# Kernel tuning notes

Hardware: AMD Instinct MI355X
Metric: run time of the kernel (lower is better)

The kernel has to match this reference:

```python
import jax, jax.numpy as jnp
import numpy as np
from jax import lax

HEADS = 4
DIM_HEAD = 32
IH = IW = 64
IH_RED = 32  # image_size // reduce_ratio; F.interpolate(size=int) -> square output


def dw_conv(t, w):
    # depthwise 3x3, stride 1, padding 1, NCHW; w: [C,1,3,3]
    return lax.conv_general_dilated(t, w, (1, 1), [(1, 1), (1, 1)],
                                    feature_group_count=t.shape[1],
                                    dimension_numbers=("NCHW", "OIHW", "NCHW"))


def pw_conv(t, w):
    # pointwise 1x1 conv as einsum; w: [O,C,1,1]
    return jnp.einsum("oc,bchw->bohw", w[:, :, 0, 0], t)


def resize_bilinear_ac(t, out_h, out_w):
    # bilinear, align_corners=True, t: [B,C,H,W]
    H, W = t.shape[-2], t.shape[-1]
    ys = jnp.linspace(0.0, H - 1.0, out_h)
    xs = jnp.linspace(0.0, W - 1.0, out_w)
    y0 = jnp.floor(ys).astype(jnp.int32)
    x0 = jnp.floor(xs).astype(jnp.int32)
    y1 = jnp.minimum(y0 + 1, H - 1)
    x1 = jnp.minimum(x0 + 1, W - 1)
    wy = (ys - y0).astype(t.dtype)[None, None, :, None]
    wx = (xs - x0).astype(t.dtype)[None, None, None, :]
    row = t[:, :, y0, :] * (1 - wy) + t[:, :, y1, :] * wy  # [B,C,OH,W]
    out = row[:, :, :, x0] * (1 - wx) + row[:, :, :, x1] * wx  # [B,C,OH,OW]
    return out


def to_heads(t):
    # [B, h*d, H, W] -> [B, h, H*W, d]
    B, _, H, W = t.shape
    return t.reshape(B, HEADS, DIM_HEAD, H * W).transpose(0, 1, 3, 2)


def setup_inputs() -> dict:
    key = jax.random.key(0)
    ks = jax.random.split(key, 7)
    inner = HEADS * DIM_HEAD  # 128
    return {
        "x": jax.random.normal(ks[0], (8, 256, 16, 16), jnp.float32),
        "skip": jax.random.normal(ks[1], (8, 128, 64, 64), jnp.float32),
        "dw_q": jax.random.normal(ks[2], (128, 1, 3, 3), jnp.float32) * 0.1,
        "pw_q": jax.random.normal(ks[3], (inner, 128, 1, 1), jnp.float32) * 0.05,
        "dw_kv": jax.random.normal(ks[4], (256, 1, 3, 3), jnp.float32) * 0.1,
        "pw_kv": jax.random.normal(ks[5], (2 * inner, 256, 1, 1), jnp.float32) * 0.05,
        "w_out": jax.random.normal(ks[6], (128, inner, 1, 1), jnp.float32) * 0.05,
    }


def reference(x, skip, dw_q, pw_q, dw_kv, pw_kv, w_out):
    scale = DIM_HEAD ** -0.5
    q = to_heads(pw_conv(dw_conv(skip, dw_q), pw_q))  # [B,h,4096,d]
    kv = pw_conv(dw_conv(x, dw_kv), pw_kv)            # [B,2*inner,16,16]
    k, v = jnp.split(kv, 2, axis=1)
    k = to_heads(resize_bilinear_ac(k, IH_RED, IH_RED))  # [B,h,1024,d]
    v = to_heads(resize_bilinear_ac(v, IH_RED, IH_RED))
    dots = jnp.einsum("bhqd,bhkd->bhqk", q, k) * scale
    attn = jax.nn.softmax(dots, axis=-1)
    out = jnp.einsum("bhqk,bhkd->bhqd", attn, v)  # [B,h,4096,d]
    B = out.shape[0]
    out = out.transpose(0, 1, 3, 2).reshape(B, HEADS * DIM_HEAD, IH, IW)
    return pw_conv(out, w_out)
```

## Files before the change

kernel.cpp:

```cpp
#include <hip/hip_runtime.h>
#include <hip/hip_bf16.h>

typedef __attribute__((ext_vector_type(4))) float f32x4;
typedef __attribute__((ext_vector_type(8))) short bf16x8;

#define DEV static __device__ __forceinline__

DEV int imin(int a, int b) { return a < b ? a : b; }

DEV short f2bf(float f) {
  union { float f; unsigned u; } v; v.f = f;
  unsigned r = (v.u + 0x7fffu + ((v.u >> 16) & 1u)) >> 16;
  return (short)r;
}

DEV unsigned pkbf(float lo, float hi) {
  unsigned r;
  asm("v_cvt_pk_bf16_f32 %0, %1, %2" : "=v"(r) : "v"(lo), "v"(hi));
  return r;
}

DEV bf16x8 cvt8(const float* __restrict__ p) {
  f32x4 a = *reinterpret_cast<const f32x4*>(p);
  f32x4 b = *reinterpret_cast<const f32x4*>(p + 4);
  bf16x8 r;
  r[0] = f2bf(a[0]); r[1] = f2bf(a[1]); r[2] = f2bf(a[2]); r[3] = f2bf(a[3]);
  r[4] = f2bf(b[0]); r[5] = f2bf(b[1]); r[6] = f2bf(b[2]); r[7] = f2bf(b[3]);
  return r;
}

DEV int swz(int q, int c) {
  return q * 64 + ((((c >> 1) ^ (q & 3)) << 4) | ((c & 1) << 3));
}
DEV int swz_rd(int q, int pair) {
  return q * 64 + ((pair ^ (q & 3)) << 4);
}

__global__ __launch_bounds__(256) void k_dwq(const float* __restrict__ skip,
    const float* __restrict__ dw_q, short* __restrict__ dwQ) {
  const int b = blockIdx.z, cq = blockIdx.y, y = blockIdx.x;
  __shared__ __align__(16) short T[64][40];
  const int t = threadIdx.x;
  {
    const int x = t & 63, cg = t >> 6;
    #pragma unroll
    for (int i = 0; i < 8; ++i) {
      const int cl = cg * 8 + i;
      const int c = cq * 32 + cl;
      const float* sp = skip + (b * 128 + c) * 4096;
      const float* wp = dw_q + c * 9;
      float acc = 0.f;
      #pragma unroll
      for (int ky = 0; ky < 3; ++ky) {
        const int yy = y + ky - 1;
        if (yy < 0 || yy > 63) continue;
        #pragma unroll
        for (int kx = 0; kx < 3; ++kx) {
          const int xx = x + kx - 1;
          if (xx < 0 || xx > 63) continue;
          acc += sp[yy * 64 + xx] * wp[ky * 3 + kx];
        }
      }
      T[x][cl] = f2bf(acc);
    }
  }
  __syncthreads();
  const int x2 = t >> 2, cc = t & 3;
  bf16x8 v = *reinterpret_cast<const bf16x8*>(&T[x2][cc * 8]);
  *reinterpret_cast<bf16x8*>(dwQ + (b * 4096 + y * 64 + x2) * 128 + cq * 32 + cc * 8) = v;
}

__global__ __launch_bounds__(256) void k_kvgen(const float* __restrict__ x,
    const float* __restrict__ dw_kv, const float* __restrict__ pw_kv,
    float* __restrict__ kv16) {
  const int b = blockIdx.y;
  const int pq = blockIdx.x;
  __shared__ __align__(16) short dwxT[16][264];
  const int t = threadIdx.x;
  {
    const int pl = t & 15;
    const int cg = t >> 4;
    const int py = pq, px = pl;
    for (int i = 0; i < 16; ++i) {
      const int c = cg * 16 + i;
      const float* sp = x + (b * 256 + c) * 256;
      const float* wp = dw_kv + c * 9;
      float acc = 0.f;
      #pragma unroll
      for (int ky = 0; ky < 3; ++ky) {
        const int yy = py + ky - 1;
        if (yy < 0 || yy > 15) continue;
        #pragma unroll
        for (int kx = 0; kx < 3; ++kx) {
          const int xx = px + kx - 1;
          if (xx < 0 || xx > 15) continue;
          acc += sp[yy * 16 + xx] * wp[ky * 3 + kx];
        }
      }
      dwxT[pl][c] = f2bf(acc);
    }
  }
  __syncthreads();
  const int w = t >> 6, l = t & 63, lr = l & 15, lg = l >> 4;
  f32x4 acc[4];
  #pragma unroll
  for (int ot = 0; ot < 4; ++ot) acc[ot] = f32x4{0.f, 0.f, 0.f, 0.f};
  #pragma unroll
  for (int kk = 0; kk < 8; ++kk) {
    const int c0 = kk * 32 + lg * 8;
    bf16x8 bfr = *reinterpret_cast<const bf16x8*>(&dwxT[lr][c0]);
    #pragma unroll
    for (int ot = 0; ot < 4; ++ot) {
      const int o = (w * 4 + ot) * 16 + lr;
      bf16x8 afr = cvt8(pw_kv + o * 256 + c0);
      acc[ot] = __builtin_amdgcn_mfma_f32_16x16x32_bf16(afr, bfr, acc[ot], 0, 0, 0);
    }
  }
  #pragma unroll
  for (int ot = 0; ot < 4; ++ot)
    #pragma unroll
    for (int r = 0; r < 4; ++r) {
      const int o = (w * 4 + ot) * 16 + lg * 4 + r;
      const int pix = pq * 16 + lr;
      kv16[(b * 256 + o) * 256 + pix] = acc[ot][r];
    }
}

DEV float bilin16(const float* __restrict__ p, int key) {
  const int oy = key >> 5, ox = key & 31;
  const float s = 15.f / 31.f;
  const float syf = oy * s, sxf = ox * s;
  const int y0 = (int)syf, x0 = (int)sxf;
  const int y1 = imin(y0 + 1, 15), x1 = imin(x0 + 1, 15);
  const float wy = syf - (float)y0, wx = sxf - (float)x0;
  const float r0 = p[y0 * 16 + x0] * (1.f - wx) + p[y0 * 16 + x1] * wx;
  const float r1 = p[y1 * 16 + x0] * (1.f - wx) + p[y1 * 16 + x1] * wx;
  return r0 * (1.f - wy) + r1 * wy;
}

__global__ __launch_bounds__(256) void k_resize(const float* __restrict__ kv16,
    short* __restrict__ K, short* __restrict__ Vt) {
  const int idx = blockIdx.x * 256 + threadIdx.x;
  {
    const int d = idx & 31;
    int rest = idx >> 5;
    const int key = rest & 1023; rest >>= 10;
    const int h = rest & 3; const int b = rest >> 2;
    const int ch = h * 32 + d;
    K[idx] = f2bf(bilin16(kv16 + (b * 256 + ch) * 256, key));
  }
  {
    const int key = idx & 1023;
    int rest = idx >> 10;
    const int d = rest & 31; rest >>= 5;
    const int h = rest & 3; const int b = rest >> 2;
    const int ch = 128 + h * 32 + d;
    Vt[idx] = f2bf(bilin16(kv16 + (b * 256 + ch) * 256, key));
  }
}

__global__ __launch_bounds__(256) void k_attn(const short* __restrict__ dwQ,
    const float* __restrict__ pw_q, const short* __restrict__ Kk,
    const short* __restrict__ Vt, const float* __restrict__ w_out,
    float* __restrict__ out) {
  const int b = blockIdx.y;
  const int q0 = blockIdx.x * 32;
  const int t = threadIdx.x, h = t >> 6, l = t & 63;
  const int lr = l & 15, lg = l >> 4;
  __shared__ __align__(16) short QT[32][136];
  __shared__ __align__(16) char QS[4][2048];
  __shared__ __align__(16) char PS[4][1024];
  __shared__ __align__(16) short AT[32][136];

  {
    const int rr = t >> 4, c16 = t & 15;
    #pragma unroll
    for (int i = 0; i < 2; ++i) {
      const int q = rr + i * 16;
      bf16x8 v = *reinterpret_cast<const bf16x8*>(dwQ + (b * 4096 + q0 + q) * 128 + c16 * 8);
      *reinterpret_cast<bf16x8*>(&QT[q][c16 * 8]) = v;
    }
  }
  __syncthreads();

  {
    f32x4 aq[2][2];
    #pragma unroll
    for (int ot = 0; ot < 2; ++ot)
      #pragma unroll
      for (int qt = 0; qt < 2; ++qt) aq[ot][qt] = f32x4{0.f, 0.f, 0.f, 0.f};
    #pragma unroll
    for (int kk = 0; kk < 4; ++kk) {
      const int c0 = kk * 32 + lg * 8;
      bf16x8 bfr[2];
      #pragma unroll
      for (int qt = 0; qt < 2; ++qt)
        bfr[qt] = *reinterpret_cast<const bf16x8*>(&QT[qt * 16 + lr][c0]);
      #pragma unroll
      for (int ot = 0; ot < 2; ++ot) {
        bf16x8 afr = cvt8(pw_q + ((h * 2 + ot) * 16 + lr) * 128 + c0);
        #pragma unroll
        for (int qt = 0; qt < 2; ++qt)
          aq[ot][qt] = __builtin_amdgcn_mfma_f32_16x16x32_bf16(afr, bfr[qt], aq[ot][qt], 0, 0, 0);
      }
    }
    const float qs = 0.25505403f;
    #pragma unroll
    for (int ot = 0; ot < 2; ++ot)
      #pragma unroll
      for (int qt = 0; qt < 2; ++qt) {
        unsigned d0 = pkbf(aq[ot][qt][0] * qs, aq[ot][qt][1] * qs);
        unsigned d1 = pkbf(aq[ot][qt][2] * qs, aq[ot][qt][3] * qs);
        const int q = qt * 16 + lr, c = ot * 4 + lg;
        *reinterpret_cast<unsigned long long*>(QS[h] + swz(q, c)) =
            ((unsigned long long)d1 << 32) | d0;
      }
  }
  asm volatile("s_waitcnt lgkmcnt(0)" ::: "memory");
  __builtin_amdgcn_sched_barrier(0);
  bf16x8 qf[2];
  #pragma unroll
  for (int qt = 0; qt < 2; ++qt) {
    const int q = qt * 16 + lr;
    qf[qt] = *reinterpret_cast<const bf16x8*>(QS[h] + swz_rd(q, lg));
  }
  __builtin_amdgcn_sched_barrier(0);

  const short* Kb = Kk + (b * 4 + h) * 32768;
  const short* Vb = Vt + (b * 4 + h) * 32768;
  f32x4 oacc[2][2];
  float ls[2];
  #pragma unroll
  for (int qt = 0; qt < 2; ++qt) {
    oacc[qt][0] = f32x4{0.f, 0.f, 0.f, 0.f};
    oacc[qt][1] = f32x4{0.f, 0.f, 0.f, 0.f};
    ls[qt] = 0.f;
  }
  for (int kc = 0; kc < 1024; kc += 32) {
    bf16x8 kf[2], vf[2];
    #pragma unroll
    for (int tt = 0; tt < 2; ++tt) {
      kf[tt] = *reinterpret_cast<const bf16x8*>(Kb + (kc + tt * 16 + lr) * 32 + lg * 8);
      vf[tt] = *reinterpret_cast<const bf16x8*>(Vb + (tt * 16 + lr) * 1024 + kc + lg * 8);
    }
    #pragma unroll
    for (int qt = 0; qt < 2; ++qt) {
      const f32x4 z = f32x4{0.f, 0.f, 0.f, 0.f};
      f32x4 s0 = __builtin_amdgcn_mfma_f32_16x16x32_bf16(kf[0], qf[qt], z, 0, 0, 0);
      f32x4 s1 = __builtin_amdgcn_mfma_f32_16x16x32_bf16(kf[1], qf[qt], z, 0, 0, 0);
      float p0[4], p1[4];
      #pragma unroll
      for (int r = 0; r < 4; ++r) {
        p0[r] = __builtin_amdgcn_exp2f(s0[r]);
        p1[r] = __builtin_amdgcn_exp2f(s1[r]);
      }
      ls[qt] += ((p0[0] + p0[1]) + (p0[2] + p0[3])) + ((p1[0] + p1[1]) + (p1[2] + p1[3]));
      unsigned a0 = pkbf(p0[0], p0[1]), a1 = pkbf(p0[2], p0[3]);
      unsigned b0 = pkbf(p1[0], p1[1]), b1 = pkbf(p1[2], p1[3]);
      *reinterpret_cast<unsigned long long*>(PS[h] + swz(lr, lg)) =
          ((unsigned long long)a1 << 32) | a0;
      *reinterpret_cast<unsigned long long*>(PS[h] + swz(lr, lg + 4)) =
          ((unsigned long long)b1 << 32) | b0;
      asm volatile("s_waitcnt lgkmcnt(0)" ::: "memory");
      __builtin_amdgcn_sched_barrier(0);
      bf16x8 pf = *reinterpret_cast<const bf16x8*>(PS[h] + swz_rd(lr, lg));
      __builtin_amdgcn_sched_barrier(0);
      oacc[qt][0] = __builtin_amdgcn_mfma_f32_16x16x32_bf16(pf, vf[0], oacc[qt][0], 0, 0, 0);
      oacc[qt][1] = __builtin_amdgcn_mfma_f32_16x16x32_bf16(pf, vf[1], oacc[qt][1], 0, 0, 0);
    }
  }

  #pragma unroll
  for (int qt = 0; qt < 2; ++qt) {
    float s = ls[qt];
    s += __shfl_xor(s, 16);
    s += __shfl_xor(s, 32);
    const float inv = 1.f / s;
    #pragma unroll
    for (int r = 0; r < 4; ++r) {
      const float invr = __shfl(inv, lg * 4 + r);
      const int q = qt * 16 + lg * 4 + r;
      #pragma unroll
      for (int tt = 0; tt < 2; ++tt)
        AT[q][h * 32 + tt * 16 + lr] = f2bf(oacc[qt][tt][r] * invr);
    }
  }
  __syncthreads();

  f32x4 ao[2][2];
  #pragma unroll
  for (int jt = 0; jt < 2; ++jt)
    #pragma unroll
    for (int qt = 0; qt < 2; ++qt) ao[jt][qt] = f32x4{0.f, 0.f, 0.f, 0.f};
  #pragma unroll
  for (int kk = 0; kk < 4; ++kk) {
    const int c0 = kk * 32 + lg * 8;
    bf16x8 bfr[2];
    #pragma unroll
    for (int qt = 0; qt < 2; ++qt)
      bfr[qt] = *reinterpret_cast<const bf16x8*>(&AT[qt * 16 + lr][c0]);
    #pragma unroll
    for (int jt = 0; jt < 2; ++jt) {
      bf16x8 afr = cvt8(w_out + ((h * 2 + jt) * 16 + lr) * 128 + c0);
      #pragma unroll
      for (int qt = 0; qt < 2; ++qt)
        ao[jt][qt] = __builtin_amdgcn_mfma_f32_16x16x32_bf16(afr, bfr[qt], ao[jt][qt], 0, 0, 0);
    }
  }
  #pragma unroll
  for (int jt = 0; jt < 2; ++jt)
    #pragma unroll
    for (int qt = 0; qt < 2; ++qt)
      #pragma unroll
      for (int r = 0; r < 4; ++r) {
        const int j = (h * 2 + jt) * 16 + lg * 4 + r;
        out[(b * 128 + j) * 4096 + q0 + qt * 16 + lr] = ao[jt][qt][r];
      }
}

extern "C" void kernel_launch(void* const* d_in, const int* in_sizes, int n_in,
                              void* d_out, int out_size, void* d_ws, size_t ws_size,
                              hipStream_t stream) {
  const float* x     = (const float*)d_in[0];
  const float* skip  = (const float*)d_in[1];
  const float* dw_q  = (const float*)d_in[2];
  const float* pw_q  = (const float*)d_in[3];
  const float* dw_kv = (const float*)d_in[4];
  const float* pw_kv = (const float*)d_in[5];
  const float* w_out = (const float*)d_in[6];
  float* out = (float*)d_out;
  (void)in_sizes; (void)n_in; (void)out_size; (void)ws_size;

  char* wsb = (char*)d_ws;
  short* dwQ  = (short*)(wsb);
  float* kv16 = (float*)(wsb + (size_t)(8u << 20));
  short* K    = (short*)(wsb + (size_t)(10u << 20));
  short* Vt   = (short*)(wsb + (size_t)(12u << 20));

  k_dwq<<<dim3(64, 4, 8), dim3(256), 0, stream>>>(skip, dw_q, dwQ);
  k_kvgen<<<dim3(16, 8), dim3(256), 0, stream>>>(x, dw_kv, pw_kv, kv16);
  k_resize<<<dim3(4096), dim3(256), 0, stream>>>(kv16, K, Vt);
  k_attn<<<dim3(128, 8), dim3(256), 0, stream>>>(dwQ, pw_q, K, Vt, w_out, out);
}
```

Before: 204.4 us.

## Permute K/V storage so MFMA outputs feed next MFMA directly from registers

The resize kernel now writes K and V in a permuted order (sigma over the head dim and key index). This lets the Q projection and the softmax probabilities be packed straight from MFMA accumulators into the B/A operands of the next MFMA, removing the LDS round trip, the waitcnt and the sched barriers in the attention inner loop. Separately, the kv-generation kernel doubles its block size to 512 threads, so each thread does half the depthwise channels and output tiles. The risk is in the permutation: if it does not exactly match the accumulator register layout, the dot products and outputs will be wrong.

Result: faster. 194.2 us (-5.0%).

```diff
diff --git a/kernel.cpp b/kernel.cpp
--- a/kernel.cpp
+++ b/kernel.cpp
@@ -3,6 +3,7 @@
 
 typedef __attribute__((ext_vector_type(4))) float f32x4;
 typedef __attribute__((ext_vector_type(8))) short bf16x8;
+typedef __attribute__((ext_vector_type(4))) unsigned u32x4;
 
 #define DEV static __device__ __forceinline__
 
@@ -29,12 +30,7 @@
   return r;
 }
 
-DEV int swz(int q, int c) {
-  return q * 64 + ((((c >> 1) ^ (q & 3)) << 4) | ((c & 1) << 3));
-}
-DEV int swz_rd(int q, int pair) {
-  return q * 64 + ((pair ^ (q & 3)) << 4);
-}
+DEV int sigma(int s) { return ((s & 4) << 2) | ((s >> 3) << 2) | (s & 3); }
 
 __global__ __launch_bounds__(256) void k_dwq(const float* __restrict__ skip,
     const float* __restrict__ dw_q, short* __restrict__ dwQ) {
@@ -70,7 +66,7 @@
   *reinterpret_cast<bf16x8*>(dwQ + (b * 4096 + y * 64 + x2) * 128 + cq * 32 + cc * 8) = v;
 }
 
-__global__ __launch_bounds__(256) void k_kvgen(const float* __restrict__ x,
+__global__ __launch_bounds__(512) void k_kvgen(const float* __restrict__ x,
     const float* __restrict__ dw_kv, const float* __restrict__ pw_kv,
     float* __restrict__ kv16) {
   const int b = blockIdx.y;
@@ -81,8 +77,9 @@
     const int pl = t & 15;
     const int cg = t >> 4;
     const int py = pq, px = pl;
-    for (int i = 0; i < 16; ++i) {
-      const int c = cg * 16 + i;
+    #pragma unroll
+    for (int i = 0; i < 8; ++i) {
+      const int c = cg * 8 + i;
       const float* sp = x + (b * 256 + c) * 256;
       const float* wp = dw_kv + c * 9;
       float acc = 0.f;
@@ -102,25 +99,25 @@
   }
   __syncthreads();
   const int w = t >> 6, l = t & 63, lr = l & 15, lg = l >> 4;
-  f32x4 acc[4];
-  #pragma unroll
-  for (int ot = 0; ot < 4; ++ot) acc[ot] = f32x4{0.f, 0.f, 0.f, 0.f};
+  f32x4 acc[2];
+  #pragma unroll
+  for (int ot = 0; ot < 2; ++ot) acc[ot] = f32x4{0.f, 0.f, 0.f, 0.f};
   #pragma unroll
   for (int kk = 0; kk < 8; ++kk) {
     const int c0 = kk * 32 + lg * 8;
     bf16x8 bfr = *reinterpret_cast<const bf16x8*>(&dwxT[lr][c0]);
     #pragma unroll
-    for (int ot = 0; ot < 4; ++ot) {
-      const int o = (w * 4 + ot) * 16 + lr;
+    for (int ot = 0; ot < 2; ++ot) {
+      const int o = (w * 2 + ot) * 16 + lr;
       bf16x8 afr = cvt8(pw_kv + o * 256 + c0);
       acc[ot] = __builtin_amdgcn_mfma_f32_16x16x32_bf16(afr, bfr, acc[ot], 0, 0, 0);
     }
   }
   #pragma unroll
-  for (int ot = 0; ot < 4; ++ot)
+  for (int ot = 0; ot < 2; ++ot)
     #pragma unroll
     for (int r = 0; r < 4; ++r) {
-      const int o = (w * 4 + ot) * 16 + lg * 4 + r;
+      const int o = (w * 2 + ot) * 16 + lg * 4 + r;
       const int pix = pq * 16 + lr;
       kv16[(b * 256 + o) * 256 + pix] = acc[ot][r];
     }
@@ -139,37 +136,36 @@
 }
 
 __global__ __launch_bounds__(256) void k_resize(const float* __restrict__ kv16,
-    short* __restrict__ K, short* __restrict__ Vt) {
+    short* __restrict__ Kp, short* __restrict__ Vp) {
   const int idx = blockIdx.x * 256 + threadIdx.x;
   {
-    const int d = idx & 31;
+    const int pos = idx & 31;
     int rest = idx >> 5;
     const int key = rest & 1023; rest >>= 10;
     const int h = rest & 3; const int b = rest >> 2;
-    const int ch = h * 32 + d;
-    K[idx] = f2bf(bilin16(kv16 + (b * 256 + ch) * 256, key));
-  }
-  {
-    const int key = idx & 1023;
+    const int ch = h * 32 + sigma(pos);
+    Kp[idx] = f2bf(bilin16(kv16 + (b * 256 + ch) * 256, key));
+  }
+  {
+    const int keypos = idx & 1023;
     int rest = idx >> 10;
     const int d = rest & 31; rest >>= 5;
     const int h = rest & 3; const int b = rest >> 2;
+    const int key = (keypos & ~31) | sigma(keypos & 31);
     const int ch = 128 + h * 32 + d;
-    Vt[idx] = f2bf(bilin16(kv16 + (b * 256 + ch) * 256, key));
+    Vp[idx] = f2bf(bilin16(kv16 + (b * 256 + ch) * 256, key));
   }
 }
 
 __global__ __launch_bounds__(256) void k_attn(const short* __restrict__ dwQ,
-    const float* __restrict__ pw_q, const short* __restrict__ Kk,
-    const short* __restrict__ Vt, const float* __restrict__ w_out,
+    const float* __restrict__ pw_q, const short* __restrict__ Kp,
+    const short* __restrict__ Vp, const float* __restrict__ w_out,
     float* __restrict__ out) {
   const int b = blockIdx.y;
   const int q0 = blockIdx.x * 32;
   const int t = threadIdx.x, h = t >> 6, l = t & 63;
   const int lr = l & 15, lg = l >> 4;
   __shared__ __align__(16) short QT[32][136];
-  __shared__ __align__(16) char QS[4][2048];
-  __shared__ __align__(16) char PS[4][1024];
   __shared__ __align__(16) short AT[32][136];
 
   {
@@ -183,6 +179,7 @@
   }
   __syncthreads();
 
+  bf16x8 qf[2];
   {
     f32x4 aq[2][2];
     #pragma unroll
@@ -206,28 +203,18 @@
     }
     const float qs = 0.25505403f;
     #pragma unroll
-    for (int ot = 0; ot < 2; ++ot)
-      #pragma unroll
-      for (int qt = 0; qt < 2; ++qt) {
-        unsigned d0 = pkbf(aq[ot][qt][0] * qs, aq[ot][qt][1] * qs);
-        unsigned d1 = pkbf(aq[ot][qt][2] * qs, aq[ot][qt][3] * qs);
-        const int q = qt * 16 + lr, c = ot * 4 + lg;
-        *reinterpret_cast<unsigned long long*>(QS[h] + swz(q, c)) =
-            ((unsigned long long)d1 << 32) | d0;
-      }
-  }
-  asm volatile("s_waitcnt lgkmcnt(0)" ::: "memory");
-  __builtin_amdgcn_sched_barrier(0);
-  bf16x8 qf[2];
-  #pragma unroll
-  for (int qt = 0; qt < 2; ++qt) {
-    const int q = qt * 16 + lr;
-    qf[qt] = *reinterpret_cast<const bf16x8*>(QS[h] + swz_rd(q, lg));
-  }
-  __builtin_amdgcn_sched_barrier(0);
-
-  const short* Kb = Kk + (b * 4 + h) * 32768;
-  const short* Vb = Vt + (b * 4 + h) * 32768;
+    for (int qt = 0; qt < 2; ++qt) {
+      u32x4 qw;
+      qw[0] = pkbf(aq[0][qt][0] * qs, aq[0][qt][1] * qs);
+      qw[1] = pkbf(aq[0][qt][2] * qs, aq[0][qt][3] * qs);
+      qw[2] = pkbf(aq[1][qt][0] * qs, aq[1][qt][1] * qs);
+      qw[3] = pkbf(aq[1][qt][2] * qs, aq[1][qt][3] * qs);
+      qf[qt] = *reinterpret_cast<bf16x8*>(&qw);
+    }
+  }
+
+  const short* Kb = Kp + (b * 4 + h) * 32768;
+  const short* Vb = Vp + (b * 4 + h) * 32768;
   f32x4 oacc[2][2];
   float ls[2];
   #pragma unroll
@@ -255,16 +242,12 @@
         p1[r] = __builtin_amdgcn_exp2f(s1[r]);
       }
       ls[qt] += ((p0[0] + p0[1]) + (p0[2] + p0[3])) + ((p1[0] + p1[1]) + (p1[2] + p1[3]));
-      unsigned a0 = pkbf(p0[0], p0[1]), a1 = pkbf(p0[2], p0[3]);
-      unsigned b0 = pkbf(p1[0], p1[1]), b1 = pkbf(p1[2], p1[3]);
-      *reinterpret_cast<unsigned long long*>(PS[h] + swz(lr, lg)) =
-          ((unsigned long long)a1 << 32) | a0;
-      *reinterpret_cast<unsigned long long*>(PS[h] + swz(lr, lg + 4)) =
-          ((unsigned long long)b1 << 32) | b0;
-      asm volatile("s_waitcnt lgkmcnt(0)" ::: "memory");
-      __builtin_amdgcn_sched_barrier(0);
-      bf16x8 pf = *reinterpret_cast<const bf16x8*>(PS[h] + swz_rd(lr, lg));
-      __builtin_amdgcn_sched_barrier(0);
+      u32x4 pw;
+      pw[0] = pkbf(p0[0], p0[1]);
+      pw[1] = pkbf(p0[2], p0[3]);
+      pw[2] = pkbf(p1[0], p1[1]);
+      pw[3] = pkbf(p1[2], p1[3]);
+      bf16x8 pf = *reinterpret_cast<bf16x8*>(&pw);
       oacc[qt][0] = __builtin_amdgcn_mfma_f32_16x16x32_bf16(pf, vf[0], oacc[qt][0], 0, 0, 0);
       oacc[qt][1] = __builtin_amdgcn_mfma_f32_16x16x32_bf16(pf, vf[1], oacc[qt][1], 0, 0, 0);
     }
@@ -334,11 +317,11 @@
   char* wsb = (char*)d_ws;
   short* dwQ  = (short*)(wsb);
   float* kv16 = (float*)(wsb + (size_t)(8u << 20));
-  short* K    = (short*)(wsb + (size_t)(10u << 20));
-  short* Vt   = (short*)(wsb + (size_t)(12u << 20));
+  short* Kp   = (short*)(wsb + (size_t)(10u << 20));
+  short* Vp   = (short*)(wsb + (size_t)(12u << 20));
 
   k_dwq<<<dim3(64, 4, 8), dim3(256), 0, stream>>>(skip, dw_q, dwQ);
-  k_kvgen<<<dim3(16, 8), dim3(256), 0, stream>>>(x, dw_kv, pw_kv, kv16);
-  k_resize<<<dim3(4096), dim3(256), 0, stream>>>(kv16, K, Vt);
-  k_attn<<<dim3(128, 8), dim3(256), 0, stream>>>(dwQ, pw_q, K, Vt, w_out, out);
-}
+  k_kvgen<<<dim3(16, 8), dim3(512), 0, stream>>>(x, dw_kv, pw_kv, kv16);
+  k_resize<<<dim3(4096), dim3(256), 0, stream>>>(kv16, Kp, Vp);
+  k_attn<<<dim3(128, 8), dim3(256), 0, stream>>>(dwQ, pw_q, Kp, Vp, w_out, out);
+}
```
